# Performance work log

Measured on AMD Instinct MI355X. Metric: run time of the kernel, lower is better.

## Reference

```python
import jax, jax.numpy as jnp
import numpy as np

WINDOW_SIZES = [4, 8, 12]
BN_EPS = 1e-5


def conv1x1(x, w, b):
    # x: [B,C,H,W], w: [O,C], b: [O]
    return jnp.einsum('bchw,oc->bohw', x, w) + b[None, :, None, None]


def bnorm(x, gamma, beta, mean, var):
    inv = gamma * jax.lax.rsqrt(var + BN_EPS)
    return (x - mean[None, :, None, None]) * inv[None, :, None, None] + beta[None, :, None, None]


def shift5(x):
    # ShiftConv2d1 depthwise fixed-weight conv == 4-direction zero-padded shift + identity
    b, c, H, W = x.shape
    g = c // 5
    p = jnp.pad(x, ((0, 0), (0, 0), (1, 1), (1, 1)))
    return jnp.concatenate([
        p[:, 0 * g:1 * g, 1:-1, 2:],    # kernel[1,2]: x[i, j+1]
        p[:, 1 * g:2 * g, 1:-1, :-2],   # kernel[1,0]: x[i, j-1]
        p[:, 2 * g:3 * g, 2:, 1:-1],    # kernel[2,1]: x[i+1, j]
        p[:, 3 * g:4 * g, :-2, 1:-1],   # kernel[0,1]: x[i-1, j]
        p[:, 4 * g:, 1:-1, 1:-1],       # kernel[1,1]: identity
    ], axis=1)


def lfe(x, w0, b0, w1, b1):
    y = jax.nn.relu(conv1x1(shift5(x), w0, b0))
    return conv1x1(shift5(y), w1, b1)


def win_part(x, ws):
    # [B,C,H,W] -> [B*nh*nw, ws*ws, C]
    b, c, H, W = x.shape
    x = x.reshape(b, c, H // ws, ws, W // ws, ws)
    return x.transpose(0, 2, 4, 3, 5, 1).reshape(b * (H // ws) * (W // ws), ws * ws, c)


def win_merge(y, ws, b, H, W):
    # [B*nh*nw, ws*ws, C] -> [B,C,H,W]
    c = y.shape[-1]
    y = y.reshape(b, H // ws, W // ws, ws, ws, c)
    return y.transpose(0, 5, 1, 3, 2, 4).reshape(b, c, H, W)


def gmsa_first(x, pi_w, pi_b, bn_g, bn_b, bn_m, bn_v, po_w, po_b):
    b, c, H, W = x.shape
    xp = bnorm(conv1x1(x, pi_w, pi_b), bn_g, bn_b, bn_m, bn_v)
    ch = 2 * c // 3
    ys, atns = [], []
    for i, ws in enumerate(WINDOW_SIZES):
        x_ = xp[:, i * ch:(i + 1) * ch]
        x_ = jnp.roll(x_, (-(ws // 2), -(ws // 2)), axis=(2, 3))
        qv = win_part(x_, ws)                      # [nw, ws*ws, 2*cc]
        cc = ch // 2
        q, v = qv[..., :cc], qv[..., cc:]
        atn = jax.nn.softmax(q @ q.transpose(0, 2, 1), axis=-1)
        y_ = win_merge(atn @ v, ws, b, H, W)
        y_ = jnp.roll(y_, (ws // 2, ws // 2), axis=(2, 3))
        ys.append(y_)
        atns.append(atn)
    return conv1x1(jnp.concatenate(ys, axis=1), po_w, po_b), atns


def gmsa_shared(x, atns, pi_w, pi_b, bn_g, bn_b, bn_m, bn_v, po_w, po_b):
    b, c, H, W = x.shape
    xp = bnorm(conv1x1(x, pi_w, pi_b), bn_g, bn_b, bn_m, bn_v)
    ch = c // 3
    ys = []
    for i, ws in enumerate(WINDOW_SIZES):
        x_ = jnp.roll(xp[:, i * ch:(i + 1) * ch], (-(ws // 2), -(ws // 2)), axis=(2, 3))
        v = win_part(x_, ws)
        y_ = win_merge(atns[i] @ v, ws, b, H, W)
        ys.append(jnp.roll(y_, (ws // 2, ws // 2), axis=(2, 3)))
    return conv1x1(jnp.concatenate(ys, axis=1), po_w, po_b)


def setup_inputs() -> dict:
    key = jax.random.key(0)
    ks = jax.random.split(key, 20)
    B, C, H, W = 4, 60, 384, 384
    E = 2 * C  # exp_ratio=2 hidden width
    s = 0.05

    def rn(k, shape):
        return jax.random.normal(k, shape, dtype=jnp.float32) * s

    return {
        'x': jax.random.normal(ks[0], (B, C, H, W), dtype=jnp.float32),
        # LFE 0
        'lfe0_w0': rn(ks[1], (E, C)), 'lfe0_b0': jnp.zeros((E,), jnp.float32),
        'lfe0_w1': rn(ks[2], (C, E)), 'lfe0_b1': jnp.zeros((C,), jnp.float32),
        # GMSA 0 (calc_attn=True): project_inp C->2C, BN(2C), project_out C->C
        'g0_pi_w': rn(ks[3], (2 * C, C)), 'g0_pi_b': jnp.zeros((2 * C,), jnp.float32),
        'g0_bn_g': jnp.ones((2 * C,), jnp.float32), 'g0_bn_b': jnp.zeros((2 * C,), jnp.float32),
        'g0_bn_m': jnp.zeros((2 * C,), jnp.float32), 'g0_bn_v': jnp.ones((2 * C,), jnp.float32),
        'g0_po_w': rn(ks[4], (C, C)), 'g0_po_b': jnp.zeros((C,), jnp.float32),
        # LFE 1
        'lfe1_w0': rn(ks[5], (E, C)), 'lfe1_b0': jnp.zeros((E,), jnp.float32),
        'lfe1_w1': rn(ks[6], (C, E)), 'lfe1_b1': jnp.zeros((C,), jnp.float32),
        # GMSA 1 (calc_attn=False): project_inp C->C, BN(C), project_out C->C
        'g1_pi_w': rn(ks[7], (C, C)), 'g1_pi_b': jnp.zeros((C,), jnp.float32),
        'g1_bn_g': jnp.ones((C,), jnp.float32), 'g1_bn_b': jnp.zeros((C,), jnp.float32),
        'g1_bn_m': jnp.zeros((C,), jnp.float32), 'g1_bn_v': jnp.ones((C,), jnp.float32),
        'g1_po_w': rn(ks[8], (C, C)), 'g1_po_b': jnp.zeros((C,), jnp.float32),
    }


def reference(x, lfe0_w0, lfe0_b0, lfe0_w1, lfe0_b1,
              g0_pi_w, g0_pi_b, g0_bn_g, g0_bn_b, g0_bn_m, g0_bn_v, g0_po_w, g0_po_b,
              lfe1_w0, lfe1_b0, lfe1_w1, lfe1_b1,
              g1_pi_w, g1_pi_b, g1_bn_g, g1_bn_b, g1_bn_m, g1_bn_v, g1_po_w, g1_po_b):
    # depth 0
    x = lfe(x, lfe0_w0, lfe0_b0, lfe0_w1, lfe0_b1) + x
    y, atns = gmsa_first(x, g0_pi_w, g0_pi_b, g0_bn_g, g0_bn_b, g0_bn_m, g0_bn_v, g0_po_w, g0_po_b)
    x = y + x
    # shared depth 1 (reuses attention maps)
    x = lfe(x, lfe1_w0, lfe1_b0, lfe1_w1, lfe1_b1) + x
    y = gmsa_shared(x, atns, g1_pi_w, g1_pi_b, g1_bn_g, g1_bn_b, g1_bn_m, g1_bn_v, g1_po_w, g1_po_b)
    return y + x
```

## Files before the change

### kernel.cpp

```cpp
#include <hip/hip_runtime.h>
#include <math.h>

constexpr int B_ = 4, C_ = 60, H_ = 384, W_ = 384;
constexpr int HW_ = H_ * W_;
constexpr int NC_ = B_ * C_ * HW_;
constexpr int NE_ = B_ * 120 * HW_;

typedef __attribute__((ext_vector_type(8))) short short8;
typedef __attribute__((ext_vector_type(4))) float f32x4;
typedef __attribute__((ext_vector_type(4))) unsigned short u16x4;

__device__ __forceinline__ unsigned short f2b(float f) {
    unsigned u = __builtin_bit_cast(unsigned, f);
    unsigned r = (u + 0x7fff + ((u >> 16) & 1)) >> 16;
    return (unsigned short)r;
}
__device__ __forceinline__ float b2f(unsigned short s) {
    return __builtin_bit_cast(float, (unsigned)s << 16);
}

__device__ __forceinline__ int xcd_swz(int bid, int nwg) {
    const int q = nwg >> 3, r = nwg & 7;
    const int xcd = bid & 7, off = bid >> 3;
    return (xcd < r ? xcd * (q + 1) : r * (q + 1) + (xcd - r) * q) + off;
}

struct PrepJobs {
    const float* src[8];
    unsigned short* dst[8];
    int cin[8];
    int cout[8];
};

__global__ __launch_bounds__(256) void prep_all(PrepJobs J)
{
    int bid = blockIdx.x;
    #pragma unroll 1
    for (int j = 0; j < 8; ++j) {
        const int KP = J.cin[j]  > 64 ? 128 : 64;
        const int MP = J.cout[j] > 64 ? 128 : 64;
        const int nb = MP * KP / 256;
        if (bid < nb) {
            const int i = bid * 256 + threadIdx.x;
            const int o = i / KP, c = i - o * KP;
            const float v = (o < J.cout[j] && c < J.cin[j]) ? J.src[j][o * J.cin[j] + c] : 0.f;
            J.dst[j][o * KP + (c ^ ((o & 7) << 3))] = f2b(v);
            return;
        }
        bid -= nb;
    }
}

struct ABJobs {
    const float* bias[8];
    const float* g[8];
    const float* bb[8];
    const float* m[8];
    const float* v[8];
    float* dst[8];
    int cout[8];
};

__global__ __launch_bounds__(256) void prep_ab(ABJobs J)
{
    const int j = blockIdx.x;
    const int n = J.cout[j];
    for (int o = threadIdx.x; o < n; o += 256) {
        float A = 1.f, Bv = J.bias[j][o];
        if (J.g[j]) {
            const float s = J.g[j][o] * rsqrtf(J.v[j][o] + 1e-5f);
            A  = s;
            Bv = (Bv - J.m[j][o]) * s + J.bb[j][o];
        }
        J.dst[j][o]     = A;
        J.dst[j][n + o] = Bv;
    }
}

template<int KP>
__device__ __forceinline__ int lds_off(int px, int cb) {
    return px * (KP * 2) + (cb ^ ((px & 7) << 4) ^ (((px >> 3) & 1) << 6));
}

template<int CIN, int COUT, int GSH, bool SRCB, bool RELU, bool RESID,
         bool RESIDB, bool OUTB>
__global__ __launch_bounds__(256, 4)
void conv_g(const void* __restrict__ in_, const unsigned short* __restrict__ wp,
            const float* __restrict__ AB,
            const void* __restrict__ resid_, void* __restrict__ out_)
{
    constexpr int KP  = CIN  > 64 ? 128 : 64;
    constexpr int MP  = COUT > 64 ? 128 : 64;
    constexpr int NNT = MP / 16;
    constexpr int KBL = KP / 32;
    __shared__ __align__(16) char xlds[128 * KP * 2];

    const int tid = threadIdx.x;
    const int n0  = blockIdx.x * 128;
    const int b   = n0 / HW_;
    const int p0  = n0 - b * HW_;
    const int hh  = p0 / W_;
    const int ww0 = p0 - hh * W_;

    for (int task = tid; task < (KP / 2) * 16; task += 256) {
        const int oct = (task >> 4) & 15;
        const int pr  = (task & 15) | ((task >> 8) << 4);
        const int c0  = pr * 2;
        const int s0  = oct * 8;

        if (c0 >= CIN) {
            #pragma unroll
            for (int i = 0; i < 8; ++i)
                *(unsigned*)(xlds + lds_off<KP>(s0 + i, c0 * 2)) = 0u;
            continue;
        }

        int dh = 0, dw = 0;
        if (GSH > 0) {
            const int grp = c0 / GSH;
            dh = (grp == 2) ? 1 : ((grp == 3) ? -1 : 0);
            dw = (grp == 0) ? 1 : ((grp == 1) ? -1 : 0);
        }
        const int h2 = hh + dh;
        const bool vh = (unsigned)h2 < (unsigned)H_;
        const long eoff = (long)(b * CIN + c0) * HW_ + h2 * W_ + ww0 + s0;

        unsigned short va[8], vb[8];
        if (vh) {
            if constexpr (SRCB) {
                const unsigned short* p = (const unsigned short*)in_;
                short8 A = *(const short8*)(p + eoff);
                short8 Bv = *(const short8*)(p + eoff + HW_);
                #pragma unroll
                for (int i = 0; i < 8; ++i) { va[i] = (unsigned short)A[i]; vb[i] = (unsigned short)Bv[i]; }
            } else {
                const float* p = (const float*)in_;
                f32x4 A0 = *(const f32x4*)(p + eoff);
                f32x4 A1 = *(const f32x4*)(p + eoff + 4);
                f32x4 B0 = *(const f32x4*)(p + eoff + HW_);
                f32x4 B1 = *(const f32x4*)(p + eoff + HW_ + 4);
                #pragma unroll
                for (int i = 0; i < 4; ++i) {
                    va[i] = f2b(A0[i]); va[i + 4] = f2b(A1[i]);
                    vb[i] = f2b(B0[i]); vb[i + 4] = f2b(B1[i]);
                }
            }
        } else {
            #pragma unroll
            for (int i = 0; i < 8; ++i) { va[i] = 0; vb[i] = 0; }
        }
        #pragma unroll
        for (int i = 0; i < 8; ++i) {
            const int px = s0 + i - dw;
            if ((unsigned)px < 128u) {
                const unsigned v = (unsigned)va[i] | ((unsigned)vb[i] << 16);
                *(unsigned*)(xlds + lds_off<KP>(px, c0 * 2)) = v;
            }
        }
        if (GSH > 0 && dw != 0) {
            const bool hndl = (dw == 1) ? (oct == 15) : (oct == 0);
            if (hndl) {
                const int px_e = (dw == 1) ? 127 : 0;
                const int w_abs = ww0 + px_e + dw;
                unsigned short ua = 0, ub = 0;
                if (vh && (unsigned)w_abs < (unsigned)W_) {
                    const long e2 = (long)(b * CIN + c0) * HW_ + h2 * W_ + w_abs;
                    if constexpr (SRCB) {
                        ua = ((const unsigned short*)in_)[e2];
                        ub = ((const unsigned short*)in_)[e2 + HW_];
                    } else {
                        ua = f2b(((const float*)in_)[e2]);
                        ub = f2b(((const float*)in_)[e2 + HW_]);
                    }
                }
                *(unsigned*)(xlds + lds_off<KP>(px_e, c0 * 2)) =
                    (unsigned)ua | ((unsigned)ub << 16);
            }
        }
    }
    __syncthreads();

    const int wv = tid >> 6, lo = tid & 15, hi = (tid & 63) >> 4;
    f32x4 acc[2][NNT];
    #pragma unroll
    for (int mt = 0; mt < 2; ++mt)
        #pragma unroll
        for (int nt = 0; nt < NNT; ++nt) acc[mt][nt] = f32x4{0.f, 0.f, 0.f, 0.f};

    #pragma unroll
    for (int kb = 0; kb < KBL; ++kb) {
        short8 a[2], bb[NNT];
        #pragma unroll
        for (int mt = 0; mt < 2; ++mt) {
            const int row = wv * 32 + mt * 16 + lo;
            a[mt] = *(const short8*)(xlds + lds_off<KP>(row, kb * 64 + hi * 16));
        }
        #pragma unroll
        for (int nt = 0; nt < NNT; ++nt) {
            const int row = nt * 16 + lo;
            bb[nt] = *(const short8*)((const char*)wp +
                      row * (KP * 2) + ((kb * 64 + hi * 16) ^ ((row & 7) << 4)));
        }
        #pragma unroll
        for (int mt = 0; mt < 2; ++mt)
            #pragma unroll
            for (int nt = 0; nt < NNT; ++nt)
                acc[mt][nt] = __builtin_amdgcn_mfma_f32_16x16x32_bf16(
                    a[mt], bb[nt], acc[mt][nt], 0, 0, 0);
    }

    #pragma unroll
    for (int mt = 0; mt < 2; ++mt) {
        const int px0 = p0 + wv * 32 + mt * 16 + hi * 4;
        #pragma unroll
        for (int nt = 0; nt < NNT; ++nt) {
            const int ch = nt * 16 + lo;
            if (ch < COUT) {
                const long oi = (long)(b * COUT + ch) * HW_ + px0;
                float v[4];
                f32x4 rf;
                u16x4 rb;
                if (RESID) {
                    if (RESIDB) rb = *(const u16x4*)((const unsigned short*)resid_ + oi);
                    else        rf = *(const f32x4*)((const float*)resid_ + oi);
                }
                #pragma unroll
                for (int r = 0; r < 4; ++r) {
                    float t = fmaf(acc[mt][nt][r], AB[ch], AB[COUT + ch]);
                    if (RELU) t = fmaxf(t, 0.f);
                    if (RESID) t += RESIDB ? b2f(rb[r]) : rf[r];
                    v[r] = t;
                }
                if (OUTB) {
                    u16x4 o4;
                    #pragma unroll
                    for (int r = 0; r < 4; ++r) o4[r] = f2b(v[r]);
                    *(u16x4*)((unsigned short*)out_ + oi) = o4;
                } else {
                    *(f32x4*)((float*)out_ + oi) = f32x4{v[0], v[1], v[2], v[3]};
                }
            }
        }
    }
}

template<bool RESIDB, bool OUTB>
__global__ __launch_bounds__(256, 4)
void conv_g2(const unsigned short* __restrict__ in_,
             const unsigned short* __restrict__ wp,
             const float* __restrict__ AB,
             const void* __restrict__ resid_, void* __restrict__ out_)
{
    constexpr int COUT = 60;
    constexpr int NNT  = 4;
    __shared__ __align__(16) char xlds[2][128 * 128];

    const int tid = threadIdx.x;
    const int n0  = blockIdx.x * 128;
    const int b   = n0 / HW_;
    const int p0  = n0 - b * HW_;
    const int hh  = p0 / W_;
    const int ww0 = p0 - hh * W_;

    auto h_load = [&](int task, int h, short8& A, short8& Bv, unsigned& edge) {
        const int oct = (task >> 5) & 15;
        const int pr  = task & 31;
        const int c0g = h * 64 + pr * 2;
        A = short8{0,0,0,0,0,0,0,0}; Bv = A; edge = 0;
        if (c0g >= 120) return;
        const int grp = c0g / 24;
        const int dh = (grp == 2) ? 1 : ((grp == 3) ? -1 : 0);
        const int dw = (grp == 0) ? 1 : ((grp == 1) ? -1 : 0);
        const int h2 = hh + dh;
        const bool vh = (unsigned)h2 < (unsigned)H_;
        const int s0 = oct * 8;
        const long eoff = (long)(b * 120 + c0g) * HW_ + h2 * W_ + ww0 + s0;
        if (vh) {
            A  = *(const short8*)(in_ + eoff);
            Bv = *(const short8*)(in_ + eoff + HW_);
        }
        if (dw != 0) {
            const bool hndl = (dw == 1) ? (oct == 15) : (oct == 0);
            if (hndl) {
                const int px_e = (dw == 1) ? 127 : 0;
                const int w_abs = ww0 + px_e + dw;
                if (vh && (unsigned)w_abs < (unsigned)W_) {
                    const long e2 = (long)(b * 120 + c0g) * HW_ + h2 * W_ + w_abs;
                    edge = (unsigned)in_[e2] | ((unsigned)in_[e2 + HW_] << 16);
                }
            }
        }
    };
    auto h_write = [&](int task, int h, short8 A, short8 Bv, unsigned edge) {
        const int oct = (task >> 5) & 15;
        const int pr  = task & 31;
        const int c0g = h * 64 + pr * 2;
        const int cb  = pr * 4;
        const int s0  = oct * 8;
        int dw = 0;
        if (c0g < 120) {
            const int grp = c0g / 24;
            dw = (grp == 0) ? 1 : ((grp == 1) ? -1 : 0);
        }
        #pragma unroll
        for (int j = 0; j < 8; ++j) {
            const int px = s0 + j - dw;
            if ((unsigned)px < 128u) {
                const unsigned v = (unsigned)(unsigned short)A[j] |
                                   ((unsigned)(unsigned short)Bv[j] << 16);
                *(unsigned*)(xlds[h] + lds_off<64>(px, cb)) = v;
            }
        }
        if (dw != 0) {
            const bool hndl = (dw == 1) ? (oct == 15) : (oct == 0);
            if (hndl) {
                const int px_e = (dw == 1) ? 127 : 0;
                *(unsigned*)(xlds[h] + lds_off<64>(px_e, cb)) = edge;
            }
        }
    };

    {
        short8 A0, B0, A1, B1; unsigned e0, e1;
        h_load(tid,       0, A0, B0, e0);
        h_load(tid + 256, 0, A1, B1, e1);
        h_write(tid,       0, A0, B0, e0);
        h_write(tid + 256, 0, A1, B1, e1);
    }
    __syncthreads();

    short8 pA0, pB0, pA1, pB1; unsigned pe0, pe1;
    h_load(tid,       1, pA0, pB0, pe0);
    h_load(tid + 256, 1, pA1, pB1, pe1);

    const int wv = tid >> 6, lo = tid & 15, hi = (tid & 63) >> 4;
    f32x4 acc[2][NNT];
    #pragma unroll
    for (int mt = 0; mt < 2; ++mt)
        #pragma unroll
        for (int nt = 0; nt < NNT; ++nt) acc[mt][nt] = f32x4{0.f, 0.f, 0.f, 0.f};

    #pragma unroll
    for (int kb = 0; kb < 2; ++kb) {
        short8 a[2], bb[NNT];
        #pragma unroll
        for (int mt = 0; mt < 2; ++mt) {
            const int row = wv * 32 + mt * 16 + lo;
            a[mt] = *(const short8*)(xlds[0] + lds_off<64>(row, kb * 64 + hi * 16));
        }
        #pragma unroll
        for (int nt = 0; nt < NNT; ++nt) {
            const int row = nt * 16 + lo;
            bb[nt] = *(const short8*)((const char*)wp +
                      row * 256 + ((kb * 64 + hi * 16) ^ ((row & 7) << 4)));
        }
        #pragma unroll
        for (int mt = 0; mt < 2; ++mt)
            #pragma unroll
            for (int nt = 0; nt < NNT; ++nt)
                acc[mt][nt] = __builtin_amdgcn_mfma_f32_16x16x32_bf16(
                    a[mt], bb[nt], acc[mt][nt], 0, 0, 0);
    }

    h_write(tid,       1, pA0, pB0, pe0);
    h_write(tid + 256, 1, pA1, pB1, pe1);
    __syncthreads();

    #pragma unroll
    for (int kb = 0; kb < 2; ++kb) {
        const int kbg = 2 + kb;
        short8 a[2], bb[NNT];
        #pragma unroll
        for (int mt = 0; mt < 2; ++mt) {
            const int row = wv * 32 + mt * 16 + lo;
            a[mt] = *(const short8*)(xlds[1] + lds_off<64>(row, kb * 64 + hi * 16));
        }
        #pragma unroll
        for (int nt = 0; nt < NNT; ++nt) {
            const int row = nt * 16 + lo;
            bb[nt] = *(const short8*)((const char*)wp +
                      row * 256 + ((kbg * 64 + hi * 16) ^ ((row & 7) << 4)));
        }
        #pragma unroll
        for (int mt = 0; mt < 2; ++mt)
            #pragma unroll
            for (int nt = 0; nt < NNT; ++nt)
                acc[mt][nt] = __builtin_amdgcn_mfma_f32_16x16x32_bf16(
                    a[mt], bb[nt], acc[mt][nt], 0, 0, 0);
    }

    #pragma unroll
    for (int mt = 0; mt < 2; ++mt) {
        const int px0 = p0 + wv * 32 + mt * 16 + hi * 4;
        #pragma unroll
        for (int nt = 0; nt < NNT; ++nt) {
            const int ch = nt * 16 + lo;
            if (ch < COUT) {
                const long oi = (long)(b * COUT + ch) * HW_ + px0;
                float v[4];
                f32x4 rf;
                u16x4 rb;
                if (RESIDB) rb = *(const u16x4*)((const unsigned short*)resid_ + oi);
                else        rf = *(const f32x4*)((const float*)resid_ + oi);
                #pragma unroll
                for (int r = 0; r < 4; ++r) {
                    float t = fmaf(acc[mt][nt][r], AB[ch], AB[COUT + ch]);
                    t += RESIDB ? b2f(rb[r]) : rf[r];
                    v[r] = t;
                }
                u16x4 o4;
                #pragma unroll
                for (int r = 0; r < 4; ++r) o4[r] = f2b(v[r]);
                *(u16x4*)((unsigned short*)out_ + oi) = o4;
            }
        }
    }
}

template<int WS, int WPB>
__global__ __launch_bounds__(256)
void attn_m(const unsigned short* __restrict__ qsrc, int qC, int qbase,
            const unsigned short* __restrict__ vsrc, int vC, int vbase,
            unsigned short* __restrict__ out, int obase)
{
    constexpr int P     = WS * WS;
    constexpr int NMT   = P / 16;
    constexpr int S     = WS / 2;
    constexpr int WGX   = W_ / WS;
    constexpr int WGY   = H_ / WS;
    constexpr int NWIN  = WGY * WGX;
    constexpr int QP    = 40;
    constexpr int KP2   = ((P + 31) / 32) * 32;
    constexpr int VP    = KP2 + 8;
    constexpr int KB2   = KP2 / 32;
    constexpr int TILES = WPB * NMT;

    __shared__ __align__(16) unsigned short Qs[WPB * P * QP];
    __shared__ __align__(16) unsigned short VTs[WPB * 32 * VP];
    __shared__ __align__(16) unsigned short Ps[WPB * P * VP];
    __shared__ float rs[WPB * P];

    const int tid = threadIdx.x;
    const int blk = xcd_swz(blockIdx.x, gridDim.x);

    for (int i = tid; i < WPB * P * 6; i += 256) {
        const int row = i / 6, j = i - (i / 6) * 6;
        *(unsigned*)&Qs[row * QP + 20 + 2 * j] = 0u;
    }
    for (int i = tid; i < WPB * 12 * (KP2 / 2); i += 256) {
        const int rr = i / (KP2 / 2), j = i - rr * (KP2 / 2);
        const int win = rr / 12, ch = 20 + (rr - (rr / 12) * 12);
        *(unsigned*)&VTs[(win * 32 + ch) * VP + 2 * j] = 0u;
    }
    if constexpr (KP2 > P) {
        for (int i = tid; i < WPB * 20 * ((KP2 - P) / 2); i += 256) {
            const int rr = i / ((KP2 - P) / 2), j = i - rr * ((KP2 - P) / 2);
            const int win = rr / 20, ch = rr - (rr / 20) * 20;
            *(unsigned*)&VTs[(win * 32 + ch) * VP + P + 2 * j] = 0u;
        }
        for (int i = tid; i < WPB * P * ((KP2 - P) / 2); i += 256) {
            const int row = i / ((KP2 - P) / 2), j = i - row * ((KP2 - P) / 2);
            *(unsigned*)&Ps[row * VP + P + 2 * j] = 0u;
        }
    }
    for (int e = tid; e < WPB * P * 20; e += 256) {
        const int win = e / (P * 20);
        const int rem = e - win * (P * 20);
        const int ch  = rem / P;
        const int pos = rem - ch * P;
        const int gw  = blk * WPB + win;
        const int b   = gw / NWIN;
        const int rwin = gw - b * NWIN;
        const int wh = rwin / WGX, ww = rwin - (rwin / WGX) * WGX;
        const int pr = pos / WS,  pc = pos - (pos / WS) * WS;
        int hs = wh * WS + pr + S; if (hs >= H_) hs -= H_;
        int wd = ww * WS + pc + S; if (wd >= W_) wd -= W_;
        const long off = (long)hs * W_ + wd;
        Qs [(win * P  + pos) * QP + ch ] = qsrc[(long)(b * qC + qbase + ch) * HW_ + off];
        VTs[(win * 32 + ch ) * VP + pos] = vsrc[(long)(b * vC + vbase + ch) * HW_ + off];
    }
    __syncthreads();

    const int wv = tid >> 6, lo = tid & 15, hi = (tid & 63) >> 4;

    for (int t = wv; t < TILES; t += 4) {
        const int win = t / NMT, mt = t - (t / NMT) * NMT;
        const unsigned short* Qw = Qs + win * P * QP;
        unsigned short* Pw = Ps + win * P * VP;

        const short8 af = *(const short8*)(Qw + (mt * 16 + lo) * QP + hi * 8);
        f32x4 a1[NMT];
        #pragma unroll
        for (int nt = 0; nt < NMT; ++nt) a1[nt] = f32x4{0.f, 0.f, 0.f, 0.f};
        #pragma unroll
        for (int nt = 0; nt < NMT; ++nt) {
            const short8 bf = *(const short8*)(Qw + (nt * 16 + lo) * QP + hi * 8);
            a1[nt] = __builtin_amdgcn_mfma_f32_16x16x32_bf16(af, bf, a1[nt], 0, 0, 0);
        }
        float psum[4] = {0.f, 0.f, 0.f, 0.f};
        #pragma unroll
        for (int nt = 0; nt < NMT; ++nt) {
            #pragma unroll
            for (int r = 0; r < 4; ++r) {
                const float p = __expf(a1[nt][r]);
                psum[r] += p;
                Pw[(mt * 16 + hi * 4 + r) * VP + nt * 16 + lo] = f2b(p);
            }
        }
        #pragma unroll
        for (int r = 0; r < 4; ++r) {
            psum[r] += __shfl_xor(psum[r], 1);
            psum[r] += __shfl_xor(psum[r], 2);
            psum[r] += __shfl_xor(psum[r], 4);
            psum[r] += __shfl_xor(psum[r], 8);
        }
        if (lo == 0) {
            #pragma unroll
            for (int r = 0; r < 4; ++r)
                rs[win * P + mt * 16 + hi * 4 + r] = psum[r];
        }
    }
    __syncthreads();

    for (int t = wv; t < TILES; t += 4) {
        const int win = t / NMT, qt = t - (t / NMT) * NMT;
        const unsigned short* Vw = VTs + win * 32 * VP;
        const unsigned short* Pw = Ps + win * P * VP;

        f32x4 a2[2];
        a2[0] = f32x4{0.f, 0.f, 0.f, 0.f};
        a2[1] = f32x4{0.f, 0.f, 0.f, 0.f};
        #pragma unroll
        for (int kb = 0; kb < KB2; ++kb) {
            const short8 bf = *(const short8*)(Pw + (qt * 16 + lo) * VP + kb * 32 + hi * 8);
            #pragma unroll
            for (int m2 = 0; m2 < 2; ++m2) {
                const short8 af = *(const short8*)(Vw + (m2 * 16 + lo) * VP + kb * 32 + hi * 8);
                a2[m2] = __builtin_amdgcn_mfma_f32_16x16x32_bf16(af, bf, a2[m2], 0, 0, 0);
            }
        }
        const int gw = blk * WPB + win;
        const int b  = gw / NWIN;
        const int rwin = gw - b * NWIN;
        const int wh = rwin / WGX, ww = rwin - (rwin / WGX) * WGX;

        const int row = qt * 16 + lo;
        const float inv = 1.f / rs[win * P + row];
        const int pr = row / WS, pc = row - (row / WS) * WS;
        int hs = wh * WS + pr + S; if (hs >= H_) hs -= H_;
        int wd = ww * WS + pc + S; if (wd >= W_) wd -= W_;
        const long pbase = (long)(b * 60 + obase) * HW_ + (long)hs * W_ + wd;
        #pragma unroll
        for (int m2 = 0; m2 < 2; ++m2) {
            #pragma unroll
            for (int r = 0; r < 4; ++r) {
                const int ch = m2 * 16 + hi * 4 + r;
                if (ch < 20)
                    out[pbase + (long)ch * HW_] = f2b(a2[m2][r] * inv);
            }
        }
    }
}

extern "C" void kernel_launch(void* const* d_in, const int* in_sizes, int n_in,
                              void* d_out, int out_size, void* d_ws, size_t ws_size,
                              hipStream_t stream)
{
    const float* x     = (const float*)d_in[0];
    const float* l0w0  = (const float*)d_in[1];
    const float* l0b0  = (const float*)d_in[2];
    const float* l0w1  = (const float*)d_in[3];
    const float* l0b1  = (const float*)d_in[4];
    const float* g0piw = (const float*)d_in[5];
    const float* g0pib = (const float*)d_in[6];
    const float* g0bng = (const float*)d_in[7];
    const float* g0bnb = (const float*)d_in[8];
    const float* g0bnm = (const float*)d_in[9];
    const float* g0bnv = (const float*)d_in[10];
    const float* g0pow = (const float*)d_in[11];
    const float* g0pob = (const float*)d_in[12];
    const float* l1w0  = (const float*)d_in[13];
    const float* l1b0  = (const float*)d_in[14];
    const float* l1w1  = (const float*)d_in[15];
    const float* l1b1  = (const float*)d_in[16];
    const float* g1piw = (const float*)d_in[17];
    const float* g1pib = (const float*)d_in[18];
    const float* g1bng = (const float*)d_in[19];
    const float* g1bnb = (const float*)d_in[20];
    const float* g1bnm = (const float*)d_in[21];
    const float* g1bnv = (const float*)d_in[22];
    const float* g1pow = (const float*)d_in[23];
    const float* g1pob = (const float*)d_in[24];

    unsigned short* HID = (unsigned short*)d_ws;
    unsigned short* XPB = HID + NE_;
    unsigned short* XP1 = XPB + NE_;
    unsigned short* YS1 = XP1 + NC_;
    unsigned short* CCB = YS1 + NC_;
    unsigned short* WP  = CCB + NC_;
    float*          ABF = (float*)(WP + 53248);
    float* OUTF  = (float*)d_out;
    unsigned short* YS0 = (unsigned short*)d_out;

    unsigned short* W1  = WP;
    unsigned short* W2  = WP + 8192;
    unsigned short* W3  = WP + 16384;
    unsigned short* W5  = WP + 24576;
    unsigned short* W6  = WP + 28672;
    unsigned short* W7  = WP + 36864;
    unsigned short* W8  = WP + 45056;
    unsigned short* W10 = WP + 49152;

    float* AB1  = ABF;
    float* AB2  = ABF + 240;
    float* AB3  = ABF + 360;
    float* AB5  = ABF + 600;
    float* AB6  = ABF + 720;
    float* AB7  = ABF + 960;
    float* AB8  = ABF + 1080;
    float* AB10 = ABF + 1200;

    PrepJobs J;
    J.src[0]=l0w0;  J.dst[0]=W1;  J.cin[0]=60;  J.cout[0]=120;
    J.src[1]=l0w1;  J.dst[1]=W2;  J.cin[1]=120; J.cout[1]=60;
    J.src[2]=g0piw; J.dst[2]=W3;  J.cin[2]=60;  J.cout[2]=120;
    J.src[3]=g0pow; J.dst[3]=W5;  J.cin[3]=60;  J.cout[3]=60;
    J.src[4]=l1w0;  J.dst[4]=W6;  J.cin[4]=60;  J.cout[4]=120;
    J.src[5]=l1w1;  J.dst[5]=W7;  J.cin[5]=120; J.cout[5]=60;
    J.src[6]=g1piw; J.dst[6]=W8;  J.cin[6]=60;  J.cout[6]=60;
    J.src[7]=g1pow; J.dst[7]=W10; J.cin[7]=60;  J.cout[7]=60;
    prep_all<<<208, 256, 0, stream>>>(J);

    ABJobs A;
    for (int j = 0; j < 8; ++j) { A.g[j]=nullptr; A.bb[j]=nullptr; A.m[j]=nullptr; A.v[j]=nullptr; }
    A.bias[0]=l0b0;  A.dst[0]=AB1;  A.cout[0]=120;
    A.bias[1]=l0b1;  A.dst[1]=AB2;  A.cout[1]=60;
    A.bias[2]=g0pib; A.dst[2]=AB3;  A.cout[2]=120; A.g[2]=g0bng; A.bb[2]=g0bnb; A.m[2]=g0bnm; A.v[2]=g0bnv;
    A.bias[3]=g0pob; A.dst[3]=AB5;  A.cout[3]=60;
    A.bias[4]=l1b0;  A.dst[4]=AB6;  A.cout[4]=120;
    A.bias[5]=l1b1;  A.dst[5]=AB7;  A.cout[5]=60;
    A.bias[6]=g1pib; A.dst[6]=AB8;  A.cout[6]=60;  A.g[6]=g1bng; A.bb[6]=g1bnb; A.m[6]=g1bnm; A.v[6]=g1bnv;
    A.bias[7]=g1pob; A.dst[7]=AB10; A.cout[7]=60;
    prep_ab<<<8, 256, 0, stream>>>(A);

    dim3 blk(256);
    dim3 gconv(B_ * HW_ / 128);

    conv_g<60,120,12,false,true,false,false,true><<<gconv,blk,0,stream>>>(
        x, W1, AB1, nullptr, HID);
    conv_g2<false,true><<<gconv,blk,0,stream>>>(HID, W2, AB2, x, CCB);
    conv_g<60,120,0,true,false,false,false,true><<<gconv,blk,0,stream>>>(
        CCB, W3, AB3, nullptr, XPB);
    attn_m<4,4><<<dim3(9216),blk,0,stream>>>(XPB,120,0,   XPB,120,20,  YS0, 0);
    attn_m<8,1><<<dim3(9216),blk,0,stream>>>(XPB,120,40,  XPB,120,60,  YS0,20);
    attn_m<12,1><<<dim3(4096),blk,0,stream>>>(XPB,120,80, XPB,120,100, YS0,40);
    conv_g<60,60,0,true,false,true,true,true><<<gconv,blk,0,stream>>>(
        YS0, W5, AB5, CCB, CCB);
    conv_g<60,120,12,true,true,false,false,true><<<gconv,blk,0,stream>>>(
        CCB, W6, AB6, nullptr, HID);
    conv_g2<true,true><<<gconv,blk,0,stream>>>(HID, W7, AB7, CCB, CCB);
    conv_g<60,60,0,true,false,false,false,true><<<gconv,blk,0,stream>>>(
        CCB, W8, AB8, nullptr, XP1);
    attn_m<4,4><<<dim3(9216),blk,0,stream>>>(XPB,120,0,  XP1,60,0,  YS1, 0);
    attn_m<8,1><<<dim3(9216),blk,0,stream>>>(XPB,120,40, XP1,60,20, YS1,20);
    attn_m<12,1><<<dim3(4096),blk,0,stream>>>(XPB,120,80,XP1,60,40, YS1,40);
    conv_g<60,60,0,true,false,true,true,false><<<gconv,blk,0,stream>>>(
        YS1, W10, AB10, CCB, OUTF);
}
```

Measured before the change: 989.0 us.

## Fuse second LFE conv with following GMSA input projection via LDS

Merges the shifted second LFE 1x1 conv (with residual) and the subsequent project_inp+BN conv into one kernel. The intermediate activation tile is staged in LDS as bf16 and consumed directly by a second MFMA GEMM, which removes one kernel launch and the global re-read of CCB. The intermediate is still written to global because later stages need it. The extra LDS buffer cuts the occupancy hint from 4 to 3 blocks per CU and adds a block-wide sync.

Result: no change. 997.6 us (+0.9%).

```diff
diff --git a/kernel.cpp b/kernel.cpp
--- a/kernel.cpp
+++ b/kernel.cpp
@@ -244,16 +244,21 @@
     }
 }
 
-template<bool RESIDB, bool OUTB>
-__global__ __launch_bounds__(256, 4)
-void conv_g2(const unsigned short* __restrict__ in_,
-             const unsigned short* __restrict__ wp,
-             const float* __restrict__ AB,
-             const void* __restrict__ resid_, void* __restrict__ out_)
+template<int COUT2, bool RESIDB>
+__global__ __launch_bounds__(256, 3)
+void conv_chain2(const unsigned short* __restrict__ in_,
+                 const unsigned short* __restrict__ wp1,
+                 const float* __restrict__ AB1,
+                 const void* __restrict__ resid_,
+                 unsigned short* __restrict__ out1,
+                 const unsigned short* __restrict__ wp2,
+                 const float* __restrict__ AB2g,
+                 unsigned short* __restrict__ out2)
 {
-    constexpr int COUT = 60;
-    constexpr int NNT  = 4;
+    constexpr int MP2  = COUT2 > 64 ? 128 : 64;
+    constexpr int NNT2 = MP2 / 16;
     __shared__ __align__(16) char xlds[2][128 * 128];
+    __shared__ __align__(16) char x1lds[128 * 128];
 
     const int tid = threadIdx.x;
     const int n0  = blockIdx.x * 128;
@@ -334,30 +339,30 @@
     h_load(tid + 256, 1, pA1, pB1, pe1);
 
     const int wv = tid >> 6, lo = tid & 15, hi = (tid & 63) >> 4;
-    f32x4 acc[2][NNT];
+    f32x4 acc[2][4];
     #pragma unroll
     for (int mt = 0; mt < 2; ++mt)
         #pragma unroll
-        for (int nt = 0; nt < NNT; ++nt) acc[mt][nt] = f32x4{0.f, 0.f, 0.f, 0.f};
+        for (int nt = 0; nt < 4; ++nt) acc[mt][nt] = f32x4{0.f, 0.f, 0.f, 0.f};
 
     #pragma unroll
     for (int kb = 0; kb < 2; ++kb) {
-        short8 a[2], bb[NNT];
+        short8 a[2], bb[4];
         #pragma unroll
         for (int mt = 0; mt < 2; ++mt) {
             const int row = wv * 32 + mt * 16 + lo;
             a[mt] = *(const short8*)(xlds[0] + lds_off<64>(row, kb * 64 + hi * 16));
         }
         #pragma unroll
-        for (int nt = 0; nt < NNT; ++nt) {
+        for (int nt = 0; nt < 4; ++nt) {
             const int row = nt * 16 + lo;
-            bb[nt] = *(const short8*)((const char*)wp +
+            bb[nt] = *(const short8*)((const char*)wp1 +
                       row * 256 + ((kb * 64 + hi * 16) ^ ((row & 7) << 4)));
         }
         #pragma unroll
         for (int mt = 0; mt < 2; ++mt)
             #pragma unroll
-            for (int nt = 0; nt < NNT; ++nt)
+            for (int nt = 0; nt < 4; ++nt)
                 acc[mt][nt] = __builtin_amdgcn_mfma_f32_16x16x32_bf16(
                     a[mt], bb[nt], acc[mt][nt], 0, 0, 0);
     }
@@ -369,49 +374,101 @@
     #pragma unroll
     for (int kb = 0; kb < 2; ++kb) {
         const int kbg = 2 + kb;
-        short8 a[2], bb[NNT];
+        short8 a[2], bb[4];
         #pragma unroll
         for (int mt = 0; mt < 2; ++mt) {
             const int row = wv * 32 + mt * 16 + lo;
             a[mt] = *(const short8*)(xlds[1] + lds_off<64>(row, kb * 64 + hi * 16));
         }
         #pragma unroll
-        for (int nt = 0; nt < NNT; ++nt) {
+        for (int nt = 0; nt < 4; ++nt) {
             const int row = nt * 16 + lo;
-            bb[nt] = *(const short8*)((const char*)wp +
+            bb[nt] = *(const short8*)((const char*)wp1 +
                       row * 256 + ((kbg * 64 + hi * 16) ^ ((row & 7) << 4)));
         }
         #pragma unroll
         for (int mt = 0; mt < 2; ++mt)
             #pragma unroll
-            for (int nt = 0; nt < NNT; ++nt)
+            for (int nt = 0; nt < 4; ++nt)
                 acc[mt][nt] = __builtin_amdgcn_mfma_f32_16x16x32_bf16(
                     a[mt], bb[nt], acc[mt][nt], 0, 0, 0);
     }
 
     #pragma unroll
     for (int mt = 0; mt < 2; ++mt) {
-        const int px0 = p0 + wv * 32 + mt * 16 + hi * 4;
-        #pragma unroll
-        for (int nt = 0; nt < NNT; ++nt) {
+        const int pxl0 = wv * 32 + mt * 16 + hi * 4;
+        const int px0  = p0 + pxl0;
+        #pragma unroll
+        for (int nt = 0; nt < 4; ++nt) {
             const int ch = nt * 16 + lo;
-            if (ch < COUT) {
-                const long oi = (long)(b * COUT + ch) * HW_ + px0;
-                float v[4];
+            const bool chv = (ch < 60);
+            float v[4] = {0.f, 0.f, 0.f, 0.f};
+            if (chv) {
+                const long oi = (long)(b * 60 + ch) * HW_ + px0;
                 f32x4 rf;
                 u16x4 rb;
                 if (RESIDB) rb = *(const u16x4*)((const unsigned short*)resid_ + oi);
                 else        rf = *(const f32x4*)((const float*)resid_ + oi);
                 #pragma unroll
                 for (int r = 0; r < 4; ++r) {
-                    float t = fmaf(acc[mt][nt][r], AB[ch], AB[COUT + ch]);
+                    float t = fmaf(acc[mt][nt][r], AB1[ch], AB1[60 + ch]);
                     t += RESIDB ? b2f(rb[r]) : rf[r];
                     v[r] = t;
                 }
                 u16x4 o4;
                 #pragma unroll
                 for (int r = 0; r < 4; ++r) o4[r] = f2b(v[r]);
-                *(u16x4*)((unsigned short*)out_ + oi) = o4;
+                *(u16x4*)(out1 + oi) = o4;
+            }
+            #pragma unroll
+            for (int r = 0; r < 4; ++r)
+                *(unsigned short*)(x1lds + lds_off<64>(pxl0 + r, ch * 2)) =
+                    chv ? f2b(v[r]) : (unsigned short)0;
+        }
+    }
+    __syncthreads();
+
+    f32x4 acc2[2][NNT2];
+    #pragma unroll
+    for (int mt = 0; mt < 2; ++mt)
+        #pragma unroll
+        for (int nt = 0; nt < NNT2; ++nt) acc2[mt][nt] = f32x4{0.f, 0.f, 0.f, 0.f};
+
+    #pragma unroll
+    for (int kb = 0; kb < 2; ++kb) {
+        short8 a[2], bb[NNT2];
+        #pragma unroll
+        for (int mt = 0; mt < 2; ++mt) {
+            const int row = wv * 32 + mt * 16 + lo;
+            a[mt] = *(const short8*)(x1lds + lds_off<64>(row, kb * 64 + hi * 16));
+        }
+        #pragma unroll
+        for (int nt = 0; nt < NNT2; ++nt) {
+            const int row = nt * 16 + lo;
+            bb[nt] = *(const short8*)((const char*)wp2 +
+                      row * 128 + ((kb * 64 + hi * 16) ^ ((row & 7) << 4)));
+        }
+        #pragma unroll
+        for (int mt = 0; mt < 2; ++mt)
+            #pragma unroll
+            for (int nt = 0; nt < NNT2; ++nt)
+                acc2[mt][nt] = __builtin_amdgcn_mfma_f32_16x16x32_bf16(
+                    a[mt], bb[nt], acc2[mt][nt], 0, 0, 0);
+    }
+
+    #pragma unroll
+    for (int mt = 0; mt < 2; ++mt) {
+        const int px0 = p0 + wv * 32 + mt * 16 + hi * 4;
+        #pragma unroll
+        for (int nt = 0; nt < NNT2; ++nt) {
+            const int ch = nt * 16 + lo;
+            if (ch < COUT2) {
+                const long oi = (long)(b * COUT2 + ch) * HW_ + px0;
+                u16x4 o4;
+                #pragma unroll
+                for (int r = 0; r < 4; ++r)
+                    o4[r] = f2b(fmaf(acc2[mt][nt][r], AB2g[ch], AB2g[COUT2 + ch]));
+                *(u16x4*)(out2 + oi) = o4;
             }
         }
     }
@@ -648,9 +705,8 @@
 
     conv_g<60,120,12,false,true,false,false,true><<<gconv,blk,0,stream>>>(
         x, W1, AB1, nullptr, HID);
-    conv_g2<false,true><<<gconv,blk,0,stream>>>(HID, W2, AB2, x, CCB);
-    conv_g<60,120,0,true,false,false,false,true><<<gconv,blk,0,stream>>>(
-        CCB, W3, AB3, nullptr, XPB);
+    conv_chain2<120,false><<<gconv,blk,0,stream>>>(
+        HID, W2, AB2, x, CCB, W3, AB3, XPB);
     attn_m<4,4><<<dim3(9216),blk,0,stream>>>(XPB,120,0,   XPB,120,20,  YS0, 0);
     attn_m<8,1><<<dim3(9216),blk,0,stream>>>(XPB,120,40,  XPB,120,60,  YS0,20);
     attn_m<12,1><<<dim3(4096),blk,0,stream>>>(XPB,120,80, XPB,120,100, YS0,40);
@@ -658,9 +714,8 @@
         YS0, W5, AB5, CCB, CCB);
     conv_g<60,120,12,true,true,false,false,true><<<gconv,blk,0,stream>>>(
         CCB, W6, AB6, nullptr, HID);
-    conv_g2<true,true><<<gconv,blk,0,stream>>>(HID, W7, AB7, CCB, CCB);
-    conv_g<60,60,0,true,false,false,false,true><<<gconv,blk,0,stream>>>(
-        CCB, W8, AB8, nullptr, XP1);
+    conv_chain2<60,true><<<gconv,blk,0,stream>>>(
+        HID, W7, AB7, CCB, CCB, W8, AB8, XP1);
     attn_m<4,4><<<dim3(9216),blk,0,stream>>>(XPB,120,0,  XP1,60,0,  YS1, 0);
     attn_m<8,1><<<dim3(9216),blk,0,stream>>>(XPB,120,40, XP1,60,20, YS1,20);
     attn_m<12,1><<<dim3(4096),blk,0,stream>>>(XPB,120,80,XP1,60,40, YS1,40);
```
